# Kernel tuning notes

Measured on AMD Instinct MI355X. Metric: run time of the kernel, lower is better.

The kernel has to match this reference:

```python
import jax, jax.numpy as jnp
import numpy as np

N_NODES = 22
K_NEIGHBOR = 4
BN_EPS = 1e-5


def _conv1d(x, w):
    # x: (B, C, L), w: (O, C, 7), stride 1, padding 3
    return jax.lax.conv_general_dilated(x, w, (1,), [(3, 3)],
                                        dimension_numbers=('NCH', 'OIH', 'NCH'))


def _block(x, w, gamma, beta):
    # x: (N, B, C, L) -> conv + per-node BatchNorm (train-mode batch stats,
    # matching the original per-node loop) + ReLU + MaxPool1d(2)
    n, b, c, l = x.shape
    y = _conv1d(x.reshape(n * b, c, l), w)            # (N*B, O, L)
    o, lo = y.shape[1], y.shape[2]
    y = y.reshape(n, b, o, lo)
    mean = y.mean(axis=(1, 3), keepdims=True)
    var = y.var(axis=(1, 3), keepdims=True)
    y = (y - mean) * jax.lax.rsqrt(var + BN_EPS)
    y = y * gamma[None, None, :, None] + beta[None, None, :, None]
    y = jax.nn.relu(y)
    y = y.reshape(n, b, o, lo // 2, 2).max(axis=-1)   # MaxPool1d(2)
    return y


def _adj_matrix(feat, k):
    # feat: (B, N, D). Squared euclidean distances, k nearest (incl. self), row-normalized.
    sq = jnp.sum(feat ** 2, axis=2, keepdims=True)            # (B, N, 1)
    dist = sq + jnp.swapaxes(sq, 1, 2) - 2.0 * jnp.einsum('bnd,bmd->bnm', feat, feat)
    _, idx = jax.lax.top_k(-dist, k)                          # smallest-k indices, (B, N, k)
    adj = jax.nn.one_hot(idx, feat.shape[1], dtype=feat.dtype).sum(axis=2)
    return adj * (1.0 / k)


def setup_inputs() -> dict:
    key = jax.random.key(0)
    ks = jax.random.split(key, 20)
    B, N, T = 256, N_NODES, 2000
    f32 = jnp.float32
    inp = {
        'x': jax.random.normal(ks[0], (B, N, T), f32),
        # conv stack (shared across all electrode nodes)
        'w1': jax.random.normal(ks[1], (4, 1, 7), f32) * 0.2,
        'g1': jnp.ones((4,), f32), 'b1': jnp.zeros((4,), f32),
        'w2': jax.random.normal(ks[2], (8, 4, 7), f32) * 0.1,
        'g2': jnp.ones((8,), f32), 'b2': jnp.zeros((8,), f32),
        'w3': jax.random.normal(ks[3], (16, 8, 7), f32) * 0.1,
        'g3': jnp.ones((16,), f32), 'b3': jnp.zeros((16,), f32),
        # graph convolutions (uniform init like torch module)
        'gw1': jax.random.uniform(ks[4], (16, 32), f32, -1/np.sqrt(32), 1/np.sqrt(32)),
        'gb1': jax.random.uniform(ks[5], (1, 1, 32), f32, -1/np.sqrt(32), 1/np.sqrt(32)),
        'gw2': jax.random.uniform(ks[6], (32, 64), f32, -1/np.sqrt(64), 1/np.sqrt(64)),
        'gb2': jax.random.uniform(ks[7], (1, 1, 64), f32, -1/np.sqrt(64), 1/np.sqrt(64)),
        'gw3': jax.random.uniform(ks[8], (64, 128), f32, -1/np.sqrt(128), 1/np.sqrt(128)),
        'gb3': jax.random.uniform(ks[9], (1, 1, 128), f32, -1/np.sqrt(128), 1/np.sqrt(128)),
        # heads (stored as (in, out))
        'fw1': jax.random.normal(ks[10], (128, 64), f32) * 0.05,
        'fb1': jnp.zeros((64,), f32),
        'fw2': jax.random.normal(ks[11], (64, 4), f32) * 0.05,
        'fb2': jnp.zeros((4,), f32),
    }
    return inp


def reference(x, w1, g1, b1, w2, g2, b2, w3, g3, b3,
              gw1, gb1, gw2, gb2, gw3, gb3, fw1, fb1, fw2, fb2):
    B, N, T = x.shape
    # --- MultiChannelConv (vectorized over electrode nodes) ---
    h = jnp.transpose(x, (1, 0, 2))[:, :, None, :]   # (N, B, 1, T)
    h = _block(h, w1, g1, b1)                        # (N, B, 4, T/2)
    h = _block(h, w2, g2, b2)                        # (N, B, 8, T/4)
    h = _block(h, w3, g3, b3)                        # (N, B, 16, T/8)
    feat = h.mean(axis=-1)                           # AdaptiveAvgPool1d(1) -> (N, B, 16)
    feat = jnp.transpose(feat, (1, 0, 2))            # (B, N, 16)
    # --- adjacency from top-k nearest neighbors ---
    adj = _adj_matrix(feat, K_NEIGHBOR)              # (B, N, N)
    # --- graph convolutions ---
    x1 = jax.nn.relu(jnp.einsum('bnm,bmf->bnf', adj, feat @ gw1) + gb1)
    x2 = jax.nn.relu(jnp.einsum('bnm,bmf->bnf', adj, x1 @ gw2) + gb2)
    x3 = jax.nn.relu(jnp.einsum('bnm,bmf->bnf', adj, x2 @ gw3) + gb3)
    # mean over nodes, then MLP head
    pooled = x3.mean(axis=1)                         # (B, 128)
    out = (pooled @ fw1 + fb1) @ fw2 + fb2           # (B, nclass)
    return out
```

## Files before the change

### kernel.cpp

```cpp
#include <hip/hip_runtime.h>

#define BSZ 256
#define NND 22
#define BN_EPS 1e-5f

typedef float v2f __attribute__((ext_vector_type(2)));

__device__ __forceinline__ v2f pkfma(v2f a, v2f b, v2f c) {
  return __builtin_elementwise_fma(a, b, c);
}

template<int CIN, int COUT, int R, int SROW>
__device__ __forceinline__ void conv_coreR(
    const float (*s_in)[SROW], const float* s_w, int tid, float y[COUT][R]) {
#pragma unroll
  for (int o = 0; o < COUT; o++)
#pragma unroll
    for (int r = 0; r < R; r++) y[o][r] = 0.f;
#pragma unroll 1
  for (int c = 0; c < CIN; c++) {
    float xr[R + 6];
    if constexpr (R == 4) {
      const float4* xp = (const float4*)&s_in[c][4 * tid];
      float4 xa = xp[0], xb = xp[1];
      float2 xc = *(const float2*)&s_in[c][4 * tid + 8];
      xr[0] = xa.x; xr[1] = xa.y; xr[2] = xa.z; xr[3] = xa.w;
      xr[4] = xb.x; xr[5] = xb.y; xr[6] = xb.z; xr[7] = xb.w;
      xr[8] = xc.x; xr[9] = xc.y;
    } else {
      const float2* xp = (const float2*)&s_in[c][2 * tid];
      float2 x0 = xp[0], x1 = xp[1], x2 = xp[2], x3 = xp[3];
      xr[0] = x0.x; xr[1] = x0.y; xr[2] = x1.x; xr[3] = x1.y;
      xr[4] = x2.x; xr[5] = x2.y; xr[6] = x3.x; xr[7] = x3.y;
    }
#pragma unroll
    for (int k = 0; k < 7; k++) {
      const float4* wp = (const float4*)&s_w[(c * 7 + k) * COUT];
#pragma unroll
      for (int o4 = 0; o4 < COUT / 4; o4++) {
        float4 wv = wp[o4];
#pragma unroll
        for (int r = 0; r < R; r++) {
          y[4 * o4 + 0][r] += wv.x * xr[r + k];
          y[4 * o4 + 1][r] += wv.y * xr[r + k];
          y[4 * o4 + 2][r] += wv.z * xr[r + k];
          y[4 * o4 + 3][r] += wv.w * xr[r + k];
        }
      }
    }
  }
}

template<int CIN, int COUT, int NTH>
__device__ __forceinline__ void stage_weights(const float* __restrict__ w,
                                              float* s_w, int tid) {
  for (int i = tid; i < CIN * 7 * COUT; i += NTH) {
    int c = i / (7 * COUT), k = (i / COUT) % 7, o = i % COUT;
    s_w[i] = w[(o * CIN + c) * 7 + k];
  }
}

template<int CIN, int COUT, int LIN, int NTH, int NT, int R>
__global__ __launch_bounds__(NTH) void conv_statsR(
    const float* __restrict__ in, long sn, long sb, long sc,
    const float* __restrict__ w, float* __restrict__ part) {
  const int TILE = R * NTH;
  const int SROW = TILE + 8;
  __shared__ alignas(16) float s_in[CIN][SROW];
  __shared__ alignas(16) float s_w[CIN * 7 * COUT];
  __shared__ float s_red[2][NTH / 64][COUT];
  int tid = threadIdx.x, n = blockIdx.z, b = blockIdx.y;
  int t0 = blockIdx.x * TILE;
  const float* base = in + (long)n * sn + (long)b * sb;
  stage_weights<CIN, COUT, NTH>(w, s_w, tid);
  for (int c = 0; c < CIN; c++)
    for (int i = tid; i < TILE + 6; i += NTH) {
      int l = t0 + i - 3;
      s_in[c][i] = (l >= 0 && l < LIN) ? base[(long)c * sc + l] : 0.f;
    }
  __syncthreads();
  float y[COUT][R];
  conv_coreR<CIN, COUT, R, SROW>(s_in, s_w, tid, y);
  bool valid = (t0 + R * tid) < LIN;
  int lane = tid & 63, wv = tid >> 6;
#pragma unroll
  for (int o = 0; o < COUT; o++) {
    float s = 0.f, q = 0.f;
    if (valid) {
#pragma unroll
      for (int r = 0; r < R; r++) { s += y[o][r]; q += y[o][r] * y[o][r]; }
    }
#pragma unroll
    for (int off = 32; off > 0; off >>= 1) {
      s += __shfl_down(s, off, 64);
      q += __shfl_down(q, off, 64);
    }
    if (lane == 0) { s_red[0][wv][o] = s; s_red[1][wv][o] = q; }
  }
  __syncthreads();
  if (tid < COUT) {
    float s = 0.f, q = 0.f;
#pragma unroll
    for (int g = 0; g < NTH / 64; g++) { s += s_red[0][g][tid]; q += s_red[1][g][tid]; }
    long slot = ((long)n * NT + blockIdx.x) * BSZ + b;
    part[slot * (2 * COUT) + tid] = s;
    part[slot * (2 * COUT) + COUT + tid] = q;
  }
}

template<int C, int NSLOT, int LIN>
__global__ __launch_bounds__(256) void stats_reduce(
    const float* __restrict__ part,
    const float* __restrict__ gamma, const float* __restrict__ beta,
    float* __restrict__ scs,
    const float* __restrict__ w2, const float* __restrict__ w3,
    float* __restrict__ w2t, float* __restrict__ w3t) {
  const int V = 2 * C;
  const int GRP = 256 / V;
  int n = blockIdx.x, tid = threadIdx.x;
  int j = tid % V, g = tid / V;
  const float* p = part + (long)n * NSLOT * V;
  float s = 0.f;
  for (int sl = g; sl < NSLOT; sl += GRP) s += p[(long)sl * V + j];
  __shared__ float red[V][GRP];
  __shared__ float tot[V];
  red[j][g] = s;
  __syncthreads();
  if (tid < V) {
    float t = 0.f;
#pragma unroll
    for (int gg = 0; gg < GRP; gg++) t += red[tid][gg];
    tot[tid] = t;
  }
  __syncthreads();
  if (tid < C) {
    float cnt = (float)BSZ * (float)LIN;
    float m = tot[tid] / cnt;
    float var = tot[C + tid] / cnt - m * m;
    float istd = 1.0f / sqrtf(var + BN_EPS);
    float scl = gamma[tid] * istd;
    scs[n * 64 + tid] = scl;
    scs[n * 64 + 32 + tid] = beta[tid] - m * scl;
  }
  if (w2t != nullptr && blockIdx.x == 0) {
    if (tid < 224) {
      int c = tid / 56, k = (tid / 8) % 7, o = tid & 7;
      w2t[tid] = w2[(o * 4 + c) * 7 + k];
    }
    for (int i = tid; i < 896; i += 256) {
      int c = i / 112, k = (i / 16) % 7, o = i & 15;
      w3t[i] = w3[(o * 8 + c) * 7 + k];
    }
  }
}

__global__ __launch_bounds__(256) void fused1(
    const float* __restrict__ x,
    const float* __restrict__ w1,
    const float* __restrict__ scs1,
    const float* __restrict__ w2t,
    float* __restrict__ y2p,
    float* __restrict__ p2) {
  __shared__ alignas(16) float s_h1[5][1008];
  __shared__ float s_red[2][4][8];
  int tid = threadIdx.x, n = blockIdx.z, b = blockIdx.y;
  const float* xb = x + (long)b * (NND * 2000) + (long)n * 2000;
  if (tid < 250) {
    bool t0 = (tid == 0), tE = (tid == 249);
    float4 A = *(const float4*)&xb[t0 ? 0 : 8 * tid - 4];
    float4 B = *(const float4*)&xb[8 * tid];
    float4 C = *(const float4*)&xb[8 * tid + 4];
    float4 D = *(const float4*)&xb[tE ? 1996 : 8 * tid + 8];
    float xr[16];
    xr[0] = A.x; xr[1] = A.y; xr[2] = A.z; xr[3] = A.w;
    xr[4] = B.x; xr[5] = B.y; xr[6] = B.z; xr[7] = B.w;
    xr[8] = C.x; xr[9] = C.y; xr[10] = C.z; xr[11] = C.w;
    xr[12] = D.x; xr[13] = D.y; xr[14] = D.z; xr[15] = D.w;
    if (t0) { xr[1] = 0.f; xr[2] = 0.f; xr[3] = 0.f; }
    if (tE) { xr[12] = 0.f; xr[13] = 0.f; xr[14] = 0.f; }
    v2f yv[2][8];
#pragma unroll
    for (int oo = 0; oo < 2; oo++)
#pragma unroll
      for (int r = 0; r < 8; r++) { yv[oo][r].x = 0.f; yv[oo][r].y = 0.f; }
#pragma unroll
    for (int k = 0; k < 7; k++) {
      v2f wpA, wpB;
      wpA.x = w1[0 * 7 + k]; wpA.y = w1[1 * 7 + k];
      wpB.x = w1[2 * 7 + k]; wpB.y = w1[3 * 7 + k];
#pragma unroll
      for (int r = 0; r < 8; r++) {
        v2f xs; xs.x = xr[r + k + 1]; xs.y = xr[r + k + 1];
        yv[0][r] = pkfma(wpA, xs, yv[0][r]);
        yv[1][r] = pkfma(wpB, xs, yv[1][r]);
      }
    }
    float sc[4], sh[4];
#pragma unroll
    for (int o = 0; o < 4; o++) {
      sc[o] = scs1[n * 64 + o];
      sh[o] = scs1[n * 64 + 32 + o];
    }
#pragma unroll
    for (int oo = 0; oo < 2; oo++) {
      {
        int o = 2 * oo;
        float a0 = yv[oo][0].x * sc[o] + sh[o], a1 = yv[oo][1].x * sc[o] + sh[o];
        float a2 = yv[oo][2].x * sc[o] + sh[o], a3 = yv[oo][3].x * sc[o] + sh[o];
        float a4 = yv[oo][4].x * sc[o] + sh[o], a5 = yv[oo][5].x * sc[o] + sh[o];
        float a6 = yv[oo][6].x * sc[o] + sh[o], a7 = yv[oo][7].x * sc[o] + sh[o];
        float4 v;
        v.x = fmaxf(fmaxf(a0, a1), 0.f);
        v.y = fmaxf(fmaxf(a2, a3), 0.f);
        v.z = fmaxf(fmaxf(a4, a5), 0.f);
        v.w = fmaxf(fmaxf(a6, a7), 0.f);
        *(float4*)&s_h1[o][4 * tid + 4] = v;
      }
      {
        int o = 2 * oo + 1;
        float a0 = yv[oo][0].y * sc[o] + sh[o], a1 = yv[oo][1].y * sc[o] + sh[o];
        float a2 = yv[oo][2].y * sc[o] + sh[o], a3 = yv[oo][3].y * sc[o] + sh[o];
        float a4 = yv[oo][4].y * sc[o] + sh[o], a5 = yv[oo][5].y * sc[o] + sh[o];
        float a6 = yv[oo][6].y * sc[o] + sh[o], a7 = yv[oo][7].y * sc[o] + sh[o];
        float4 v;
        v.x = fmaxf(fmaxf(a0, a1), 0.f);
        v.y = fmaxf(fmaxf(a2, a3), 0.f);
        v.z = fmaxf(fmaxf(a4, a5), 0.f);
        v.w = fmaxf(fmaxf(a6, a7), 0.f);
        *(float4*)&s_h1[o][4 * tid + 4] = v;
      }
    }
  }
  if (tid < 4) {
    *(float4*)&s_h1[tid][0] = make_float4(0.f, 0.f, 0.f, 0.f);
    *(float4*)&s_h1[tid][1004] = make_float4(0.f, 0.f, 0.f, 0.f);
  }
  __syncthreads();
  v2f y2v[4][4];
#pragma unroll
  for (int oo = 0; oo < 4; oo++)
#pragma unroll
    for (int r = 0; r < 4; r++) { y2v[oo][r].x = 0.f; y2v[oo][r].y = 0.f; }
  if (tid < 250) {
    const float4* xp0 = (const float4*)&s_h1[0][4 * tid];
    float4 n0 = xp0[0], n1 = xp0[1], n2 = xp0[2];
#pragma unroll 1
    for (int c = 0; c < 4; c++) {
      float4 c0 = n0, c1 = n1, c2 = n2;
      const float4* xpn = (const float4*)&s_h1[c + 1][4 * tid];
      n0 = xpn[0]; n1 = xpn[1]; n2 = xpn[2];
      float xr[12];
      xr[0] = c0.x; xr[1] = c0.y; xr[2] = c0.z; xr[3] = c0.w;
      xr[4] = c1.x; xr[5] = c1.y; xr[6] = c1.z; xr[7] = c1.w;
      xr[8] = c2.x; xr[9] = c2.y; xr[10] = c2.z; xr[11] = c2.w;
#pragma unroll
      for (int k = 0; k < 7; k++) {
        float4 w0 = *(const float4*)&w2t[(c * 7 + k) * 8];
        float4 w1v = *(const float4*)&w2t[(c * 7 + k) * 8 + 4];
        v2f wp0, wp1, wp2, wp3;
        wp0.x = w0.x; wp0.y = w0.y;
        wp1.x = w0.z; wp1.y = w0.w;
        wp2.x = w1v.x; wp2.y = w1v.y;
        wp3.x = w1v.z; wp3.y = w1v.w;
#pragma unroll
        for (int r = 0; r < 4; r++) {
          v2f xs; xs.x = xr[r + k + 1]; xs.y = xr[r + k + 1];
          y2v[0][r] = pkfma(wp0, xs, y2v[0][r]);
          y2v[1][r] = pkfma(wp1, xs, y2v[1][r]);
          y2v[2][r] = pkfma(wp2, xs, y2v[2][r]);
          y2v[3][r] = pkfma(wp3, xs, y2v[3][r]);
        }
      }
    }
    long yb = ((long)n * BSZ + b) * 4000 + 2 * tid;
#pragma unroll
    for (int oo = 0; oo < 4; oo++) {
      float2 vx, vy;
      vx.x = fmaxf(y2v[oo][0].x, y2v[oo][1].x);
      vx.y = fmaxf(y2v[oo][2].x, y2v[oo][3].x);
      *(float2*)&y2p[yb + (2 * oo) * 500] = vx;
      vy.x = fmaxf(y2v[oo][0].y, y2v[oo][1].y);
      vy.y = fmaxf(y2v[oo][2].y, y2v[oo][3].y);
      *(float2*)&y2p[yb + (2 * oo + 1) * 500] = vy;
    }
  }
  int lane = tid & 63, wv = tid >> 6;
#pragma unroll
  for (int o = 0; o < 8; o++) {
    float g0 = (o & 1) ? y2v[o >> 1][0].y : y2v[o >> 1][0].x;
    float g1 = (o & 1) ? y2v[o >> 1][1].y : y2v[o >> 1][1].x;
    float g2 = (o & 1) ? y2v[o >> 1][2].y : y2v[o >> 1][2].x;
    float g3 = (o & 1) ? y2v[o >> 1][3].y : y2v[o >> 1][3].x;
    float s = g0 + g1 + g2 + g3;
    float q = g0 * g0 + g1 * g1 + g2 * g2 + g3 * g3;
#pragma unroll
    for (int off = 32; off > 0; off >>= 1) {
      s += __shfl_down(s, off, 64);
      q += __shfl_down(q, off, 64);
    }
    if (lane == 0) { s_red[0][wv][o] = s; s_red[1][wv][o] = q; }
  }
  __syncthreads();
  if (tid < 8) {
    float s = 0.f, q = 0.f;
#pragma unroll
    for (int g = 0; g < 4; g++) { s += s_red[0][g][tid]; q += s_red[1][g][tid]; }
    long slot = (long)n * BSZ + b;
    p2[slot * 16 + tid] = s;
    p2[slot * 16 + 8 + tid] = q;
  }
}

__global__ __launch_bounds__(256) void fused2(
    const float* __restrict__ y2p,
    const float* __restrict__ scs2,
    const float* __restrict__ w3t,
    float* __restrict__ y3p,
    float* __restrict__ p3) {
  __shared__ float s_red[2][4][8];
  int tid = threadIdx.x, n = blockIdx.z, b = blockIdx.y;
  int og = __builtin_amdgcn_readfirstlane(tid >> 7);
  int pt = tid & 127;
  bool valid = pt < 125;
  v2f y3v[4][4];
#pragma unroll
  for (int oo = 0; oo < 4; oo++)
#pragma unroll
    for (int r = 0; r < 4; r++) { y3v[oo][r].x = 0.f; y3v[oo][r].y = 0.f; }
  if (valid) {
    const float* yrow = y2p + ((long)n * BSZ + b) * 4000;
    bool p0 = (pt == 0), pE = (pt == 124);
    int offA = p0 ? 0 : 4 * pt - 4;
    int offB = 4 * pt;
    int offC = pE ? 496 : 4 * pt + 4;
    float4 nA = *(const float4*)&yrow[offA];
    float4 nB = *(const float4*)&yrow[offB];
    float4 nC = *(const float4*)&yrow[offC];
#pragma unroll 1
    for (int c = 0; c < 8; c++) {
      float4 A = nA, B = nB, C = nC;
      const float* nxt = yrow + (c + 1) * 500;
      nA = *(const float4*)&nxt[offA];
      nB = *(const float4*)&nxt[offB];
      nC = *(const float4*)&nxt[offC];
      float sc = scs2[n * 64 + c], sh = scs2[n * 64 + 32 + c];
      float xr[12];
      xr[0] = A.x; xr[1] = A.y; xr[2] = A.z; xr[3] = A.w;
      xr[4] = B.x; xr[5] = B.y; xr[6] = B.z; xr[7] = B.w;
      xr[8] = C.x; xr[9] = C.y; xr[10] = C.z; xr[11] = C.w;
#pragma unroll
      for (int j = 0; j < 12; j++) xr[j] = fmaxf(xr[j] * sc + sh, 0.f);
      if (p0) { xr[1] = 0.f; xr[2] = 0.f; xr[3] = 0.f; }
      if (pE) { xr[8] = 0.f; xr[9] = 0.f; xr[10] = 0.f; }
#pragma unroll
      for (int k = 0; k < 7; k++) {
        float4 w0 = *(const float4*)&w3t[(c * 7 + k) * 16 + og * 8];
        float4 w1v = *(const float4*)&w3t[(c * 7 + k) * 16 + og * 8 + 4];
        v2f wp0, wp1, wp2, wp3;
        wp0.x = w0.x; wp0.y = w0.y;
        wp1.x = w0.z; wp1.y = w0.w;
        wp2.x = w1v.x; wp2.y = w1v.y;
        wp3.x = w1v.z; wp3.y = w1v.w;
#pragma unroll
        for (int r = 0; r < 4; r++) {
          v2f xs; xs.x = xr[r + k + 1]; xs.y = xr[r + k + 1];
          y3v[0][r] = pkfma(wp0, xs, y3v[0][r]);
          y3v[1][r] = pkfma(wp1, xs, y3v[1][r]);
          y3v[2][r] = pkfma(wp2, xs, y3v[2][r]);
          y3v[3][r] = pkfma(wp3, xs, y3v[3][r]);
        }
      }
    }
    long yb = (((long)n * BSZ + b) * 16 + og * 8) * 250 + 2 * pt;
#pragma unroll
    for (int oo = 0; oo < 4; oo++) {
      float2 vx, vy;
      vx.x = fmaxf(y3v[oo][0].x, y3v[oo][1].x);
      vx.y = fmaxf(y3v[oo][2].x, y3v[oo][3].x);
      *(float2*)&y3p[yb + (2 * oo) * 250] = vx;
      vy.x = fmaxf(y3v[oo][0].y, y3v[oo][1].y);
      vy.y = fmaxf(y3v[oo][2].y, y3v[oo][3].y);
      *(float2*)&y3p[yb + (2 * oo + 1) * 250] = vy;
    }
  }
  int lane = tid & 63, wv = tid >> 6;
#pragma unroll
  for (int o = 0; o < 8; o++) {
    float g0 = (o & 1) ? y3v[o >> 1][0].y : y3v[o >> 1][0].x;
    float g1 = (o & 1) ? y3v[o >> 1][1].y : y3v[o >> 1][1].x;
    float g2 = (o & 1) ? y3v[o >> 1][2].y : y3v[o >> 1][2].x;
    float g3 = (o & 1) ? y3v[o >> 1][3].y : y3v[o >> 1][3].x;
    float s = g0 + g1 + g2 + g3;
    float q = g0 * g0 + g1 * g1 + g2 * g2 + g3 * g3;
#pragma unroll
    for (int off = 32; off > 0; off >>= 1) {
      s += __shfl_down(s, off, 64);
      q += __shfl_down(q, off, 64);
    }
    if (lane == 0) { s_red[0][wv][o] = s; s_red[1][wv][o] = q; }
  }
  __syncthreads();
  if (tid < 16) {
    int og2 = tid >> 3, o = tid & 7;
    float s = s_red[0][2 * og2][o] + s_red[0][2 * og2 + 1][o];
    float q = s_red[1][2 * og2][o] + s_red[1][2 * og2 + 1][o];
    long slot = (long)n * BSZ + b;
    p3[slot * 32 + tid] = s;
    p3[slot * 32 + 16 + tid] = q;
  }
}

__global__ __launch_bounds__(256) void feat_apply(
    const float* __restrict__ y3p,
    const float* __restrict__ scs3,
    float* __restrict__ feat) {
  int tid = threadIdx.x, n = blockIdx.z, b = blockIdx.y;
  int ch = tid >> 4, s = tid & 15;
  const float* yb = y3p + (((long)n * BSZ + b) * 16 + ch) * 250;
  float sc = scs3[n * 64 + ch], sh = scs3[n * 64 + 32 + ch];
  float acc = 0.f;
  for (int j = s; j < 125; j += 16) {
    float2 v = *(const float2*)&yb[2 * j];
    acc += fmaxf(v.x * sc + sh, 0.f) + fmaxf(v.y * sc + sh, 0.f);
  }
#pragma unroll
  for (int off = 8; off > 0; off >>= 1) acc += __shfl_down(acc, off, 16);
  if (s == 0) feat[((long)b * NND + n) * 16 + ch] = acc * (1.0f / 250.f);
}

__global__ __launch_bounds__(256) void graph_head(
    const float* __restrict__ feat,
    const float* __restrict__ gw1, const float* __restrict__ gb1,
    const float* __restrict__ gw2, const float* __restrict__ gb2,
    const float* __restrict__ gw3, const float* __restrict__ gb3,
    const float* __restrict__ fw1, const float* __restrict__ fb1,
    const float* __restrict__ fw2, const float* __restrict__ fb2,
    float* __restrict__ out) {
  int b = blockIdx.x, tid = threadIdx.x;
  __shared__ float s_feat[NND][16];
  __shared__ float s_sq[NND];
  __shared__ float s_dist[NND][NND];
  __shared__ float s_adj[NND][NND];
  __shared__ float s_x[NND][128];
  __shared__ float s_t[NND][128];
  __shared__ float s_pool[128];
  __shared__ float s_h[64];
  for (int i = tid; i < NND * 16; i += 256) s_feat[i >> 4][i & 15] = feat[b * NND * 16 + i];
  __syncthreads();
  if (tid < NND) {
    float s = 0.f;
    for (int c = 0; c < 16; c++) s += s_feat[tid][c] * s_feat[tid][c];
    s_sq[tid] = s;
  }
  __syncthreads();
  for (int i = tid; i < NND * NND; i += 256) {
    int nn = i / NND, m = i % NND;
    float d = 0.f;
    for (int c = 0; c < 16; c++) d += s_feat[nn][c] * s_feat[m][c];
    s_dist[nn][m] = s_sq[nn] + s_sq[m] - 2.f * d;
    s_adj[nn][m] = 0.f;
  }
  __syncthreads();
  if (tid < NND) {
    unsigned used = 0;
    for (int j = 0; j < 4; j++) {
      float best = 3.4e38f; int bi = 0;
      for (int m = 0; m < NND; m++)
        if (!((used >> m) & 1u) && s_dist[tid][m] < best) { best = s_dist[tid][m]; bi = m; }
      used |= 1u << bi;
      s_adj[tid][bi] = 0.25f;
    }
  }
  __syncthreads();
  for (int i = tid; i < NND * 32; i += 256) {
    int nn = i / 32, f = i % 32;
    float a = 0.f;
    for (int c = 0; c < 16; c++) a += s_feat[nn][c] * gw1[c * 32 + f];
    s_t[nn][f] = a;
  }
  __syncthreads();
  for (int i = tid; i < NND * 32; i += 256) {
    int nn = i / 32, f = i % 32;
    float a = gb1[f];
    for (int m = 0; m < NND; m++) a += s_adj[nn][m] * s_t[m][f];
    s_x[nn][f] = fmaxf(a, 0.f);
  }
  __syncthreads();
  for (int i = tid; i < NND * 64; i += 256) {
    int nn = i / 64, f = i % 64;
    float a = 0.f;
    for (int c = 0; c < 32; c++) a += s_x[nn][c] * gw2[c * 64 + f];
    s_t[nn][f] = a;
  }
  __syncthreads();
  for (int i = tid; i < NND * 64; i += 256) {
    int nn = i / 64, f = i % 64;
    float a = gb2[f];
    for (int m = 0; m < NND; m++) a += s_adj[nn][m] * s_t[m][f];
    s_x[nn][f] = fmaxf(a, 0.f);
  }
  __syncthreads();
  for (int i = tid; i < NND * 128; i += 256) {
    int nn = i / 128, f = i % 128;
    float a = 0.f;
    for (int c = 0; c < 64; c++) a += s_x[nn][c] * gw3[c * 128 + f];
    s_t[nn][f] = a;
  }
  __syncthreads();
  for (int i = tid; i < NND * 128; i += 256) {
    int nn = i / 128, f = i % 128;
    float a = gb3[f];
    for (int m = 0; m < NND; m++) a += s_adj[nn][m] * s_t[m][f];
    s_x[nn][f] = fmaxf(a, 0.f);
  }
  __syncthreads();
  if (tid < 128) {
    float a = 0.f;
    for (int m = 0; m < NND; m++) a += s_x[m][tid];
    s_pool[tid] = a * (1.0f / (float)NND);
  }
  __syncthreads();
  if (tid < 64) {
    float a = fb1[tid];
    for (int c = 0; c < 128; c++) a += s_pool[c] * fw1[c * 64 + tid];
    s_h[tid] = a;
  }
  __syncthreads();
  if (tid < 4) {
    float a = fb2[tid];
    for (int c = 0; c < 64; c++) a += s_h[c] * fw2[c * 4 + tid];
    out[b * 4 + tid] = a;
  }
}

extern "C" void kernel_launch(void* const* d_in, const int* in_sizes, int n_in,
                              void* d_out, int out_size, void* d_ws, size_t ws_size,
                              hipStream_t stream) {
  (void)in_sizes; (void)n_in; (void)out_size; (void)ws_size;
  const float* x   = (const float*)d_in[0];
  const float* w1  = (const float*)d_in[1];
  const float* g1  = (const float*)d_in[2];
  const float* b1  = (const float*)d_in[3];
  const float* w2  = (const float*)d_in[4];
  const float* g2  = (const float*)d_in[5];
  const float* b2  = (const float*)d_in[6];
  const float* w3  = (const float*)d_in[7];
  const float* g3  = (const float*)d_in[8];
  const float* b3  = (const float*)d_in[9];
  const float* gw1 = (const float*)d_in[10];
  const float* gb1 = (const float*)d_in[11];
  const float* gw2 = (const float*)d_in[12];
  const float* gb2 = (const float*)d_in[13];
  const float* gw3 = (const float*)d_in[14];
  const float* gb3 = (const float*)d_in[15];
  const float* fw1 = (const float*)d_in[16];
  const float* fb1 = (const float*)d_in[17];
  const float* fw2 = (const float*)d_in[18];
  const float* fb2 = (const float*)d_in[19];

  float* ws = (float*)d_ws;
  const long Y2 = (long)NND * BSZ * 8 * 500;
  const long Y3 = (long)NND * BSZ * 16 * 250;
  float* y2p  = ws;
  float* y3p  = y2p + Y2;
  float* feat = y3p + Y3;
  float* scs1 = feat + (long)BSZ * NND * 16;
  float* scs2 = scs1 + NND * 64;
  float* scs3 = scs2 + NND * 64;
  float* p1   = scs3 + NND * 64;
  float* p2   = p1 + (long)NND * 512 * 8;
  float* p3   = p2 + (long)NND * 256 * 16;
  float* w2t  = p3 + (long)NND * 256 * 32;
  float* w3t  = w2t + 224;

  conv_statsR<1, 4, 2000, 256, 2, 4><<<dim3(2, BSZ, NND), dim3(256), 0, stream>>>(
      x, 2000, (long)NND * 2000, 0, w1, p1);
  stats_reduce<4, 512, 2000><<<dim3(NND), dim3(256), 0, stream>>>(
      p1, g1, b1, scs1, w2, w3, w2t, w3t);
  fused1<<<dim3(1, BSZ, NND), dim3(256), 0, stream>>>(x, w1, scs1, w2t, y2p, p2);
  stats_reduce<8, 256, 1000><<<dim3(NND), dim3(256), 0, stream>>>(
      p2, g2, b2, scs2, nullptr, nullptr, nullptr, nullptr);
  fused2<<<dim3(1, BSZ, NND), dim3(256), 0, stream>>>(y2p, scs2, w3t, y3p, p3);
  stats_reduce<16, 256, 500><<<dim3(NND), dim3(256), 0, stream>>>(
      p3, g3, b3, scs3, nullptr, nullptr, nullptr, nullptr);
  feat_apply<<<dim3(1, BSZ, NND), dim3(256), 0, stream>>>(y3p, scs3, feat);
  graph_head<<<dim3(BSZ), dim3(256), 0, stream>>>(
      feat, gw1, gb1, gw2, gb2, gw3, gb3, fw1, fb1, fw2, fb2, (float*)d_out);
}
```

Baseline: 208.2 us.

## Store pooled raw conv1 output instead of recomputing conv1 in fused1

The stage-1 stats kernel now also writes the max-pooled pre-BN conv1 output to workspace. fused1 reads it back and applies scale/shift and ReLU on load, instead of recomputing conv1 from x. Pooling before the affine is only equivalent when the BN scale is non-negative, which is a correctness risk. The conv2 and conv3 weights are also staged into shared memory. This trades conv1 recompute for an extra write and read of a 4x1000 buffer per (node, batch), and reuses workspace by aliasing y3p with y1p.

```diff
diff --git a/kernel.cpp b/kernel.cpp
--- a/kernel.cpp
+++ b/kernel.cpp
@@ -20,19 +20,12 @@
 #pragma unroll 1
   for (int c = 0; c < CIN; c++) {
     float xr[R + 6];
-    if constexpr (R == 4) {
-      const float4* xp = (const float4*)&s_in[c][4 * tid];
-      float4 xa = xp[0], xb = xp[1];
-      float2 xc = *(const float2*)&s_in[c][4 * tid + 8];
-      xr[0] = xa.x; xr[1] = xa.y; xr[2] = xa.z; xr[3] = xa.w;
-      xr[4] = xb.x; xr[5] = xb.y; xr[6] = xb.z; xr[7] = xb.w;
-      xr[8] = xc.x; xr[9] = xc.y;
-    } else {
-      const float2* xp = (const float2*)&s_in[c][2 * tid];
-      float2 x0 = xp[0], x1 = xp[1], x2 = xp[2], x3 = xp[3];
-      xr[0] = x0.x; xr[1] = x0.y; xr[2] = x1.x; xr[3] = x1.y;
-      xr[4] = x2.x; xr[5] = x2.y; xr[6] = x3.x; xr[7] = x3.y;
-    }
+    const float4* xp = (const float4*)&s_in[c][4 * tid];
+    float4 xa = xp[0], xb = xp[1];
+    float2 xc = *(const float2*)&s_in[c][4 * tid + 8];
+    xr[0] = xa.x; xr[1] = xa.y; xr[2] = xa.z; xr[3] = xa.w;
+    xr[4] = xb.x; xr[5] = xb.y; xr[6] = xb.z; xr[7] = xb.w;
+    xr[8] = xc.x; xr[9] = xc.y;
 #pragma unroll
     for (int k = 0; k < 7; k++) {
       const float4* wp = (const float4*)&s_w[(c * 7 + k) * COUT];
@@ -61,9 +54,10 @@
 }
 
 template<int CIN, int COUT, int LIN, int NTH, int NT, int R>
-__global__ __launch_bounds__(NTH) void conv_statsR(
+__global__ __launch_bounds__(NTH) void conv_stats1p(
     const float* __restrict__ in, long sn, long sb, long sc,
-    const float* __restrict__ w, float* __restrict__ part) {
+    const float* __restrict__ w, float* __restrict__ part,
+    float* __restrict__ y1p) {
   const int TILE = R * NTH;
   const int SROW = TILE + 8;
   __shared__ alignas(16) float s_in[CIN][SROW];
@@ -82,6 +76,17 @@
   float y[COUT][R];
   conv_coreR<CIN, COUT, R, SROW>(s_in, s_w, tid, y);
   bool valid = (t0 + R * tid) < LIN;
+  if (valid) {
+    int p0 = (t0 + R * tid) >> 1;
+    long yb = ((long)n * BSZ + b) * 4000 + p0;
+#pragma unroll
+    for (int o = 0; o < COUT; o++) {
+      float2 v;
+      v.x = fmaxf(y[o][0], y[o][1]);
+      v.y = fmaxf(y[o][2], y[o][3]);
+      *(float2*)&y1p[yb + (long)o * 1000] = v;
+    }
+  }
   int lane = tid & 63, wv = tid >> 6;
 #pragma unroll
   for (int o = 0; o < COUT; o++) {
@@ -155,108 +160,51 @@
 }
 
 __global__ __launch_bounds__(256) void fused1(
-    const float* __restrict__ x,
-    const float* __restrict__ w1,
+    const float* __restrict__ y1p,
     const float* __restrict__ scs1,
     const float* __restrict__ w2t,
     float* __restrict__ y2p,
     float* __restrict__ p2) {
-  __shared__ alignas(16) float s_h1[5][1008];
+  __shared__ alignas(16) float s_w2[224];
   __shared__ float s_red[2][4][8];
   int tid = threadIdx.x, n = blockIdx.z, b = blockIdx.y;
-  const float* xb = x + (long)b * (NND * 2000) + (long)n * 2000;
-  if (tid < 250) {
-    bool t0 = (tid == 0), tE = (tid == 249);
-    float4 A = *(const float4*)&xb[t0 ? 0 : 8 * tid - 4];
-    float4 B = *(const float4*)&xb[8 * tid];
-    float4 C = *(const float4*)&xb[8 * tid + 4];
-    float4 D = *(const float4*)&xb[tE ? 1996 : 8 * tid + 8];
-    float xr[16];
-    xr[0] = A.x; xr[1] = A.y; xr[2] = A.z; xr[3] = A.w;
-    xr[4] = B.x; xr[5] = B.y; xr[6] = B.z; xr[7] = B.w;
-    xr[8] = C.x; xr[9] = C.y; xr[10] = C.z; xr[11] = C.w;
-    xr[12] = D.x; xr[13] = D.y; xr[14] = D.z; xr[15] = D.w;
-    if (t0) { xr[1] = 0.f; xr[2] = 0.f; xr[3] = 0.f; }
-    if (tE) { xr[12] = 0.f; xr[13] = 0.f; xr[14] = 0.f; }
-    v2f yv[2][8];
-#pragma unroll
-    for (int oo = 0; oo < 2; oo++)
-#pragma unroll
-      for (int r = 0; r < 8; r++) { yv[oo][r].x = 0.f; yv[oo][r].y = 0.f; }
-#pragma unroll
-    for (int k = 0; k < 7; k++) {
-      v2f wpA, wpB;
-      wpA.x = w1[0 * 7 + k]; wpA.y = w1[1 * 7 + k];
-      wpB.x = w1[2 * 7 + k]; wpB.y = w1[3 * 7 + k];
-#pragma unroll
-      for (int r = 0; r < 8; r++) {
-        v2f xs; xs.x = xr[r + k + 1]; xs.y = xr[r + k + 1];
-        yv[0][r] = pkfma(wpA, xs, yv[0][r]);
-        yv[1][r] = pkfma(wpB, xs, yv[1][r]);
-      }
-    }
-    float sc[4], sh[4];
-#pragma unroll
-    for (int o = 0; o < 4; o++) {
-      sc[o] = scs1[n * 64 + o];
-      sh[o] = scs1[n * 64 + 32 + o];
-    }
-#pragma unroll
-    for (int oo = 0; oo < 2; oo++) {
-      {
-        int o = 2 * oo;
-        float a0 = yv[oo][0].x * sc[o] + sh[o], a1 = yv[oo][1].x * sc[o] + sh[o];
-        float a2 = yv[oo][2].x * sc[o] + sh[o], a3 = yv[oo][3].x * sc[o] + sh[o];
-        float a4 = yv[oo][4].x * sc[o] + sh[o], a5 = yv[oo][5].x * sc[o] + sh[o];
-        float a6 = yv[oo][6].x * sc[o] + sh[o], a7 = yv[oo][7].x * sc[o] + sh[o];
-        float4 v;
-        v.x = fmaxf(fmaxf(a0, a1), 0.f);
-        v.y = fmaxf(fmaxf(a2, a3), 0.f);
-        v.z = fmaxf(fmaxf(a4, a5), 0.f);
-        v.w = fmaxf(fmaxf(a6, a7), 0.f);
-        *(float4*)&s_h1[o][4 * tid + 4] = v;
-      }
-      {
-        int o = 2 * oo + 1;
-        float a0 = yv[oo][0].y * sc[o] + sh[o], a1 = yv[oo][1].y * sc[o] + sh[o];
-        float a2 = yv[oo][2].y * sc[o] + sh[o], a3 = yv[oo][3].y * sc[o] + sh[o];
-        float a4 = yv[oo][4].y * sc[o] + sh[o], a5 = yv[oo][5].y * sc[o] + sh[o];
-        float a6 = yv[oo][6].y * sc[o] + sh[o], a7 = yv[oo][7].y * sc[o] + sh[o];
-        float4 v;
-        v.x = fmaxf(fmaxf(a0, a1), 0.f);
-        v.y = fmaxf(fmaxf(a2, a3), 0.f);
-        v.z = fmaxf(fmaxf(a4, a5), 0.f);
-        v.w = fmaxf(fmaxf(a6, a7), 0.f);
-        *(float4*)&s_h1[o][4 * tid + 4] = v;
-      }
-    }
-  }
-  if (tid < 4) {
-    *(float4*)&s_h1[tid][0] = make_float4(0.f, 0.f, 0.f, 0.f);
-    *(float4*)&s_h1[tid][1004] = make_float4(0.f, 0.f, 0.f, 0.f);
-  }
-  __syncthreads();
+  if (tid < 224) s_w2[tid] = w2t[tid];
+  __syncthreads();
+  bool valid = tid < 250;
   v2f y2v[4][4];
 #pragma unroll
   for (int oo = 0; oo < 4; oo++)
 #pragma unroll
     for (int r = 0; r < 4; r++) { y2v[oo][r].x = 0.f; y2v[oo][r].y = 0.f; }
-  if (tid < 250) {
-    const float4* xp0 = (const float4*)&s_h1[0][4 * tid];
-    float4 n0 = xp0[0], n1 = xp0[1], n2 = xp0[2];
+  if (valid) {
+    const float* yrow = y1p + ((long)n * BSZ + b) * 4000;
+    bool p0 = (tid == 0), pE = (tid == 249);
+    int offA = p0 ? 0 : 4 * tid - 4;
+    int offB = 4 * tid;
+    int offC = pE ? 996 : 4 * tid + 4;
+    float4 nA = *(const float4*)&yrow[offA];
+    float4 nB = *(const float4*)&yrow[offB];
+    float4 nC = *(const float4*)&yrow[offC];
 #pragma unroll 1
     for (int c = 0; c < 4; c++) {
-      float4 c0 = n0, c1 = n1, c2 = n2;
-      const float4* xpn = (const float4*)&s_h1[c + 1][4 * tid];
-      n0 = xpn[0]; n1 = xpn[1]; n2 = xpn[2];
+      float4 A = nA, B = nB, C = nC;
+      const float* nxt = yrow + (c + 1) * 1000;
+      nA = *(const float4*)&nxt[offA];
+      nB = *(const float4*)&nxt[offB];
+      nC = *(const float4*)&nxt[offC];
+      float sc = scs1[n * 64 + c], sh = scs1[n * 64 + 32 + c];
       float xr[12];
-      xr[0] = c0.x; xr[1] = c0.y; xr[2] = c0.z; xr[3] = c0.w;
-      xr[4] = c1.x; xr[5] = c1.y; xr[6] = c1.z; xr[7] = c1.w;
-      xr[8] = c2.x; xr[9] = c2.y; xr[10] = c2.z; xr[11] = c2.w;
+      xr[0] = A.x; xr[1] = A.y; xr[2] = A.z; xr[3] = A.w;
+      xr[4] = B.x; xr[5] = B.y; xr[6] = B.z; xr[7] = B.w;
+      xr[8] = C.x; xr[9] = C.y; xr[10] = C.z; xr[11] = C.w;
+#pragma unroll
+      for (int j = 0; j < 12; j++) xr[j] = fmaxf(xr[j] * sc + sh, 0.f);
+      if (p0) { xr[1] = 0.f; xr[2] = 0.f; xr[3] = 0.f; }
+      if (pE) { xr[8] = 0.f; xr[9] = 0.f; xr[10] = 0.f; }
 #pragma unroll
       for (int k = 0; k < 7; k++) {
-        float4 w0 = *(const float4*)&w2t[(c * 7 + k) * 8];
-        float4 w1v = *(const float4*)&w2t[(c * 7 + k) * 8 + 4];
+        float4 w0 = *(const float4*)&s_w2[(c * 7 + k) * 8];
+        float4 w1v = *(const float4*)&s_w2[(c * 7 + k) * 8 + 4];
         v2f wp0, wp1, wp2, wp3;
         wp0.x = w0.x; wp0.y = w0.y;
         wp1.x = w0.z; wp1.y = w0.w;
@@ -317,8 +265,11 @@
     const float* __restrict__ w3t,
     float* __restrict__ y3p,
     float* __restrict__ p3) {
+  __shared__ alignas(16) float s_w3[896];
   __shared__ float s_red[2][4][8];
   int tid = threadIdx.x, n = blockIdx.z, b = blockIdx.y;
+  for (int i = tid; i < 896; i += 256) s_w3[i] = w3t[i];
+  __syncthreads();
   int og = __builtin_amdgcn_readfirstlane(tid >> 7);
   int pt = tid & 127;
   bool valid = pt < 125;
@@ -354,8 +305,8 @@
       if (pE) { xr[8] = 0.f; xr[9] = 0.f; xr[10] = 0.f; }
 #pragma unroll
       for (int k = 0; k < 7; k++) {
-        float4 w0 = *(const float4*)&w3t[(c * 7 + k) * 16 + og * 8];
-        float4 w1v = *(const float4*)&w3t[(c * 7 + k) * 16 + og * 8 + 4];
+        float4 w0 = *(const float4*)&s_w3[(c * 7 + k) * 16 + og * 8];
+        float4 w1v = *(const float4*)&s_w3[(c * 7 + k) * 16 + og * 8 + 4];
         v2f wp0, wp1, wp2, wp3;
         wp0.x = w0.x; wp0.y = w0.y;
         wp1.x = w0.z; wp1.y = w0.w;
@@ -559,11 +510,11 @@
   const float* fb2 = (const float*)d_in[19];
 
   float* ws = (float*)d_ws;
-  const long Y2 = (long)NND * BSZ * 8 * 500;
-  const long Y3 = (long)NND * BSZ * 16 * 250;
-  float* y2p  = ws;
-  float* y3p  = y2p + Y2;
-  float* feat = y3p + Y3;
+  const long RSZ = (long)NND * BSZ * 4000;
+  float* y1p  = ws;
+  float* y3p  = ws;
+  float* y2p  = ws + RSZ;
+  float* feat = y2p + RSZ;
   float* scs1 = feat + (long)BSZ * NND * 16;
   float* scs2 = scs1 + NND * 64;
   float* scs3 = scs2 + NND * 64;
@@ -573,11 +524,11 @@
   float* w2t  = p3 + (long)NND * 256 * 32;
   float* w3t  = w2t + 224;
 
-  conv_statsR<1, 4, 2000, 256, 2, 4><<<dim3(2, BSZ, NND), dim3(256), 0, stream>>>(
-      x, 2000, (long)NND * 2000, 0, w1, p1);
+  conv_stats1p<1, 4, 2000, 256, 2, 4><<<dim3(2, BSZ, NND), dim3(256), 0, stream>>>(
+      x, 2000, (long)NND * 2000, 0, w1, p1, y1p);
   stats_reduce<4, 512, 2000><<<dim3(NND), dim3(256), 0, stream>>>(
       p1, g1, b1, scs1, w2, w3, w2t, w3t);
-  fused1<<<dim3(1, BSZ, NND), dim3(256), 0, stream>>>(x, w1, scs1, w2t, y2p, p2);
+  fused1<<<dim3(1, BSZ, NND), dim3(256), 0, stream>>>(y1p, scs1, w2t, y2p, p2);
   stats_reduce<8, 256, 1000><<<dim3(NND), dim3(256), 0, stream>>>(
       p2, g2, b2, scs2, nullptr, nullptr, nullptr, nullptr);
   fused2<<<dim3(1, BSZ, NND), dim3(256), 0, stream>>>(y2p, scs2, w3t, y3p, p3);
```

After: 212.3 us. Within noise of the previous version (+1.9%).
